# Kernel optimization log

Measured on AMD Instinct MI355X. Metric: run time of the kernel, lower is better.

## Reference

```python
import jax, jax.numpy as jnp
import numpy as np

N_NODES = 50000


def _gcn_conv(x, W, b, src, dst, n_nodes):
    """PyG GCNConv: add self-loops, symmetric deg^-1/2 norm, linear, aggregate, bias."""
    # add self-loops
    loop = jnp.arange(n_nodes, dtype=src.dtype)
    s = jnp.concatenate([src, loop])  # [E+N]
    d = jnp.concatenate([dst, loop])  # [E+N]
    # degree of A + I computed over targets
    deg = jax.ops.segment_sum(jnp.ones_like(d, dtype=x.dtype), d, num_segments=n_nodes)
    dinv = jnp.where(deg > 0, jax.lax.rsqrt(deg), 0.0)
    norm = dinv[s] * dinv[d]  # [E+N]
    h = x @ W  # [N, out] transform-first (in_dim >= out_dim friendly)
    msg = h[s] * norm[:, None]  # [E+N, out]
    out = jax.ops.segment_sum(msg, d, num_segments=n_nodes)
    return out + b


def setup_inputs() -> dict:
    key = jax.random.key(0)
    k1, k2, k3, k4 = jax.random.split(key, 4)
    in_dim, hidden, out_dim = 256, 128, 64
    E = 800000
    x = jax.random.normal(k1, (N_NODES, in_dim), dtype=jnp.float32)
    edge_index = jax.random.randint(k2, (2, E), 0, N_NODES, dtype=jnp.int64)
    W1 = jax.random.normal(k3, (in_dim, hidden), dtype=jnp.float32) / np.sqrt(in_dim)
    b1 = jnp.zeros((hidden,), dtype=jnp.float32)
    W2 = jax.random.normal(k4, (hidden, out_dim), dtype=jnp.float32) / np.sqrt(hidden)
    b2 = jnp.zeros((out_dim,), dtype=jnp.float32)
    return {"x": x, "edge_index": edge_index, "W1": W1, "b1": b1, "W2": W2, "b2": b2}


def reference(x, edge_index, W1, b1, W2, b2):
    src, dst = edge_index[0], edge_index[1]
    h = _gcn_conv(x, W1, b1, src, dst, N_NODES)
    h = jax.nn.relu(h)
    out = _gcn_conv(h, W2, b2, src, dst, N_NODES)
    return out
```

## Files before the change

kernel.cpp:

```cpp
#include <hip/hip_runtime.h>

#define N_NODES 50000
#define NCH 256
#define NBKT 256

typedef short bf16x8 __attribute__((ext_vector_type(8)));
typedef float f32x4 __attribute__((ext_vector_type(4)));

__device__ inline unsigned short f2bf(float f) {
    union { float f; unsigned u; } v; v.f = f;
    unsigned u = v.u;
    unsigned lsb = (u >> 16) & 1u;
    u += 0x7fffu + lsb;
    return (unsigned short)(u >> 16);
}

__device__ inline float bf2f(unsigned short h) {
    union { unsigned u; float f; } v; v.u = ((unsigned)h) << 16;
    return v.f;
}

__global__ __launch_bounds__(256) void prep(const int* __restrict__ dst,
                                            int* __restrict__ cnt, int E, int epc,
                                            const float* __restrict__ W1,
                                            const float* __restrict__ W2,
                                            unsigned short* __restrict__ B1h,
                                            unsigned short* __restrict__ B1l,
                                            unsigned short* __restrict__ B2h,
                                            unsigned short* __restrict__ B2l) {
    const int c = blockIdx.x;
    if (c < NCH) {
        __shared__ int h[NBKT];
        h[threadIdx.x] = 0;
        __syncthreads();
        const int e0 = c * epc;
        const int e1 = min(E, e0 + epc);
        for (int e = e0 + threadIdx.x; e < e1; e += 256)
            atomicAdd(&h[dst[e] >> 8], 1);
        __syncthreads();
        cnt[c * NBKT + threadIdx.x] = h[threadIdx.x];
        return;
    }
    int i = (c - NCH) * 256 + threadIdx.x;
    const float* W;
    unsigned short *Th, *Tl;
    int K, logM, idx;
    if (i < 32768) { W = W1; Th = B1h; Tl = B1l; K = 256; logM = 7; idx = i; }
    else if (i < 32768 + 8192) { W = W2; Th = B2h; Tl = B2l; K = 128; logM = 6; idx = i - 32768; }
    else return;
    const int M = 1 << logM;
    const int KS = K / 32;
    int k = idx >> logM;
    int n = idx & (M - 1);
    float v = W[idx];
    unsigned short h = f2bf(v);
    unsigned short l = f2bf(v - bf2f(h));
    int g = n >> 4, n16 = n & 15, ks = k >> 5, quad = (k >> 3) & 3, j = k & 7;
    size_t o = ((size_t)((g * KS + ks) * 64 + quad * 16 + n16)) * 8 + j;
    Th[o] = h;
    Tl[o] = l;
}

__global__ __launch_bounds__(256) void bkt_scan_chunks(const int* __restrict__ cnt,
                                                       int* __restrict__ off,
                                                       int* __restrict__ total) {
    __shared__ int sh[256];
    const int b = blockIdx.x;
    const int t = threadIdx.x;
    int v = cnt[t * NBKT + b];
    sh[t] = v;
    __syncthreads();
    for (int o = 1; o < 256; o <<= 1) {
        int u = (t >= o) ? sh[t - o] : 0;
        __syncthreads();
        sh[t] += u;
        __syncthreads();
    }
    off[t * NBKT + b] = sh[t] - v;
    if (t == 255) total[b] = sh[255];
}

__global__ __launch_bounds__(256) void bkt_scan_base(const int* __restrict__ total,
                                                     int* __restrict__ bbase,
                                                     int* __restrict__ rowptr,
                                                     int N, int E) {
    __shared__ int sh[256];
    const int t = threadIdx.x;
    int v = total[t];
    sh[t] = v;
    __syncthreads();
    for (int o = 1; o < 256; o <<= 1) {
        int u = (t >= o) ? sh[t - o] : 0;
        __syncthreads();
        sh[t] += u;
        __syncthreads();
    }
    bbase[t] = sh[t] - v;
    if (t == 255) bbase[256] = sh[255];
    if (t == 0) rowptr[N] = E;
}

__global__ __launch_bounds__(256) void bkt_scatter(const int* __restrict__ src,
                                                   const int* __restrict__ dst,
                                                   const int* __restrict__ off,
                                                   const int* __restrict__ bbase,
                                                   unsigned* __restrict__ pairs,
                                                   int E, int epc) {
    __shared__ int cur[NBKT];
    const int c = blockIdx.x;
    cur[threadIdx.x] = bbase[threadIdx.x] + off[c * NBKT + threadIdx.x];
    __syncthreads();
    const int e0 = c * epc;
    const int e1 = min(E, e0 + epc);
    for (int e = e0 + threadIdx.x; e < e1; e += 256) {
        int s = src[e];
        int d = dst[e];
        int pos = atomicAdd(&cur[d >> 8], 1);
        pairs[pos] = ((unsigned)s << 8) | (unsigned)(d & 255);
    }
}

__global__ __launch_bounds__(256) void bkt_csr(const unsigned* __restrict__ pairs,
                                               const int* __restrict__ bbase,
                                               int* __restrict__ rowptr,
                                               int* __restrict__ csr_src,
                                               float* __restrict__ dinv, int N) {
    __shared__ int lh[256];
    __shared__ int sc[256];
    __shared__ int lcur[256];
    const int b = blockIdx.x;
    const int t = threadIdx.x;
    const int ebase = bbase[b];
    const int eend = bbase[b + 1];
    const int node0 = b << 8;

    lh[t] = 0;
    __syncthreads();
    for (int e = ebase + t; e < eend; e += 256)
        atomicAdd(&lh[pairs[e] & 255u], 1);
    __syncthreads();
    int v = lh[t];
    sc[t] = v;
    __syncthreads();
    for (int o = 1; o < 256; o <<= 1) {
        int u = (t >= o) ? sc[t - o] : 0;
        __syncthreads();
        sc[t] += u;
        __syncthreads();
    }
    const int excl = sc[t] - v;
    lcur[t] = ebase + excl;
    const int node = node0 + t;
    if (node < N) {
        rowptr[node] = ebase + excl;
        dinv[node] = rsqrtf((float)(v + 1));
    }
    __syncthreads();
    for (int e = ebase + t; e < eend; e += 256) {
        unsigned p = pairs[e];
        int pos = atomicAdd(&lcur[p & 255u], 1);
        csr_src[pos] = (int)(p >> 8);
    }
}

template <int K, int M>
__global__ __launch_bounds__(M * 4) void gemm_mfma_v4(const float* __restrict__ A,
                                                      const unsigned short* __restrict__ Bfh,
                                                      const unsigned short* __restrict__ Bfl,
                                                      const float* __restrict__ dinv,
                                                      unsigned short* __restrict__ Cb, int N) {
    const int KS = K / 32;
    const int THREADS = M * 4;
    const int CPT = 512 / THREADS;
    const int PL = 64 * 40;
    const int CPAIRS = M / 32;

    __shared__ __align__(16) unsigned short Ah[2 * PL];
    __shared__ __align__(16) unsigned short Al[2 * PL];

    const int tid = threadIdx.x;
    const int wave = tid >> 6;
    const int lane = tid & 63;
    const int n16 = lane & 15;
    const int quad = lane >> 4;
    const int cpair = wave & (CPAIRS - 1);
    const int rpair = wave / CPAIRS;
    const int row0 = blockIdx.x * 64;

    bf16x8 bh[2][2], bl[2][2];
    auto loadB = [&](int ks, int par) {
#pragma unroll
        for (int ct = 0; ct < 2; ct++) {
            const int g = cpair * 2 + ct;
            const size_t o = ((size_t)(g * KS + ks) * 64 + lane) * 8;
            bh[par][ct] = *(const bf16x8*)(Bfh + o);
            bl[par][ct] = *(const bf16x8*)(Bfl + o);
        }
    };
    loadB(0, 0);

    int srow[CPT], sc4[CPT];
    const float* aptr[CPT];
#pragma unroll
    for (int p = 0; p < CPT; p++) {
        int q = p * THREADS + tid;
        srow[p] = q >> 3;
        sc4[p] = q & 7;
        int grow = row0 + srow[p];
        if (grow >= N) grow = N - 1;
        aptr[p] = A + (size_t)grow * K + sc4[p] * 4;
    }

    float4 pre[CPT];
#pragma unroll
    for (int p = 0; p < CPT; p++) pre[p] = *(const float4*)(aptr[p]);

#pragma unroll
    for (int p = 0; p < CPT; p++) {
        ushort4 h4, l4;
        unsigned short* hp = (unsigned short*)&h4;
        unsigned short* lp = (unsigned short*)&l4;
        float av[4] = {pre[p].x, pre[p].y, pre[p].z, pre[p].w};
#pragma unroll
        for (int j = 0; j < 4; j++) {
            unsigned short h = f2bf(av[j]);
            hp[j] = h;
            lp[j] = f2bf(av[j] - bf2f(h));
        }
        *(ushort4*)(Ah + srow[p] * 40 + sc4[p] * 4) = h4;
        *(ushort4*)(Al + srow[p] * 40 + sc4[p] * 4) = l4;
    }
    if (KS > 1) {
#pragma unroll
        for (int p = 0; p < CPT; p++) pre[p] = *(const float4*)(aptr[p] + 32);
    }
    __syncthreads();

    f32x4 acc[2][2] = {};

#pragma unroll
    for (int ks = 0; ks < KS; ks++) {
        const int cur = ks & 1;
        if (ks + 1 < KS) loadB(ks + 1, cur ^ 1);
#pragma unroll
        for (int rt = 0; rt < 2; rt++) {
            const int ro = cur * PL + (rpair * 32 + rt * 16 + n16) * 40 + quad * 8;
            bf16x8 ah = *(const bf16x8*)(Ah + ro);
            bf16x8 al = *(const bf16x8*)(Al + ro);
#pragma unroll
            for (int ct = 0; ct < 2; ct++) {
                acc[rt][ct] = __builtin_amdgcn_mfma_f32_16x16x32_bf16(ah, bh[cur][ct], acc[rt][ct], 0, 0, 0);
                acc[rt][ct] = __builtin_amdgcn_mfma_f32_16x16x32_bf16(ah, bl[cur][ct], acc[rt][ct], 0, 0, 0);
                acc[rt][ct] = __builtin_amdgcn_mfma_f32_16x16x32_bf16(al, bh[cur][ct], acc[rt][ct], 0, 0, 0);
            }
        }
        if (ks + 1 < KS) {
            const int nxt = (cur ^ 1) * PL;
#pragma unroll
            for (int p = 0; p < CPT; p++) {
                ushort4 h4, l4;
                unsigned short* hp = (unsigned short*)&h4;
                unsigned short* lp = (unsigned short*)&l4;
                float av[4] = {pre[p].x, pre[p].y, pre[p].z, pre[p].w};
#pragma unroll
                for (int j = 0; j < 4; j++) {
                    unsigned short h = f2bf(av[j]);
                    hp[j] = h;
                    lp[j] = f2bf(av[j] - bf2f(h));
                }
                *(ushort4*)(Ah + nxt + srow[p] * 40 + sc4[p] * 4) = h4;
                *(ushort4*)(Al + nxt + srow[p] * 40 + sc4[p] * 4) = l4;
            }
            if (ks + 2 < KS) {
#pragma unroll
                for (int p = 0; p < CPT; p++)
                    pre[p] = *(const float4*)(aptr[p] + (ks + 2) * 32);
            }
        }
        __syncthreads();
    }

#pragma unroll
    for (int rt = 0; rt < 2; rt++) {
#pragma unroll
        for (int ct = 0; ct < 2; ct++) {
            const int col = cpair * 32 + ct * 16 + n16;
            const int rbase = row0 + rpair * 32 + rt * 16 + quad * 4;
#pragma unroll
            for (int r = 0; r < 4; r++) {
                int orow = rbase + r;
                if (orow < N) {
                    Cb[(size_t)orow * M + col] = f2bf(dinv[orow] * acc[rt][ct][r]);
                }
            }
        }
    }
}

template <int K, int M>
__global__ __launch_bounds__(M * 4) void gemm_mfma_bfA(const unsigned short* __restrict__ A,
                                                       const unsigned short* __restrict__ Bfh,
                                                       const unsigned short* __restrict__ Bfl,
                                                       const float* __restrict__ dinv,
                                                       unsigned short* __restrict__ Cb, int N) {
    const int KS = K / 32;
    const int THREADS = M * 4;
    const int CPT = 256 / THREADS ? 256 / THREADS : 1;
    const int PL = 64 * 40;
    const int CPAIRS = M / 32;

    __shared__ __align__(16) unsigned short Ah[2 * PL];

    const int tid = threadIdx.x;
    const int wave = tid >> 6;
    const int lane = tid & 63;
    const int n16 = lane & 15;
    const int quad = lane >> 4;
    const int cpair = wave & (CPAIRS - 1);
    const int rpair = wave / CPAIRS;
    const int row0 = blockIdx.x * 64;

    bf16x8 bh[2][2], bl[2][2];
    auto loadB = [&](int ks, int par) {
#pragma unroll
        for (int ct = 0; ct < 2; ct++) {
            const int g = cpair * 2 + ct;
            const size_t o = ((size_t)(g * KS + ks) * 64 + lane) * 8;
            bh[par][ct] = *(const bf16x8*)(Bfh + o);
            bl[par][ct] = *(const bf16x8*)(Bfl + o);
        }
    };
    loadB(0, 0);

    const int srow = tid >> 2;
    const int sc8 = tid & 3;
    const unsigned short* aptr;
    {
        int grow = row0 + srow;
        if (grow >= N) grow = N - 1;
        aptr = A + (size_t)grow * K + sc8 * 8;
    }

    bf16x8 pre = *(const bf16x8*)(aptr);

    {
        ushort4* d0 = (ushort4*)(Ah + srow * 40 + sc8 * 8);
        ushort4 lo, hi;
        unsigned short* lp = (unsigned short*)&lo;
        unsigned short* hp = (unsigned short*)&hi;
#pragma unroll
        for (int j = 0; j < 4; j++) { lp[j] = (unsigned short)pre[j]; hp[j] = (unsigned short)pre[j + 4]; }
        d0[0] = lo;
        d0[1] = hi;
    }
    if (KS > 1) pre = *(const bf16x8*)(aptr + 32);
    __syncthreads();

    f32x4 acc[2][2] = {};

#pragma unroll
    for (int ks = 0; ks < KS; ks++) {
        const int cur = ks & 1;
        if (ks + 1 < KS) loadB(ks + 1, cur ^ 1);
#pragma unroll
        for (int rt = 0; rt < 2; rt++) {
            const int ro = cur * PL + (rpair * 32 + rt * 16 + n16) * 40 + quad * 8;
            bf16x8 ah = *(const bf16x8*)(Ah + ro);
#pragma unroll
            for (int ct = 0; ct < 2; ct++) {
                acc[rt][ct] = __builtin_amdgcn_mfma_f32_16x16x32_bf16(ah, bh[cur][ct], acc[rt][ct], 0, 0, 0);
                acc[rt][ct] = __builtin_amdgcn_mfma_f32_16x16x32_bf16(ah, bl[cur][ct], acc[rt][ct], 0, 0, 0);
            }
        }
        if (ks + 1 < KS) {
            const int nxt = (cur ^ 1) * PL;
            ushort4* d0 = (ushort4*)(Ah + nxt + srow * 40 + sc8 * 8);
            ushort4 lo, hi;
            unsigned short* lp = (unsigned short*)&lo;
            unsigned short* hp = (unsigned short*)&hi;
#pragma unroll
            for (int j = 0; j < 4; j++) { lp[j] = (unsigned short)pre[j]; hp[j] = (unsigned short)pre[j + 4]; }
            d0[0] = lo;
            d0[1] = hi;
            if (ks + 2 < KS) pre = *(const bf16x8*)(aptr + (ks + 2) * 32);
        }
        __syncthreads();
    }

#pragma unroll
    for (int rt = 0; rt < 2; rt++) {
#pragma unroll
        for (int ct = 0; ct < 2; ct++) {
            const int col = cpair * 32 + ct * 16 + n16;
            const int rbase = row0 + rpair * 32 + rt * 16 + quad * 4;
#pragma unroll
            for (int r = 0; r < 4; r++) {
                int orow = rbase + r;
                if (orow < N) {
                    Cb[(size_t)orow * M + col] = f2bf(dinv[orow] * acc[rt][ct][r]);
                }
            }
        }
    }
}

template <int M>
__global__ __launch_bounds__(256) void gather_to_bf16(const unsigned short* __restrict__ hnb,
                                                      const int* __restrict__ rowptr,
                                                      const int* __restrict__ csr_src,
                                                      const float* __restrict__ dinv,
                                                      const float* __restrict__ bias,
                                                      unsigned short* __restrict__ outp, int n) {
    const int MQ = M / 8;
    const int GPB = 256 / MQ;
    int g = blockIdx.x * GPB + threadIdx.x / MQ;
    int j = threadIdx.x % MQ;
    if (g >= n) return;

    float acc[8];
    {
        bf16x8 v = *(const bf16x8*)(hnb + (size_t)g * M + j * 8);
#pragma unroll
        for (int i = 0; i < 8; i++) acc[i] = bf2f((unsigned short)v[i]);
    }

    int e = rowptr[g];
    const int end = rowptr[g + 1];
    for (; e + 3 < end; e += 4) {
        int s0 = csr_src[e];
        int s1 = csr_src[e + 1];
        int s2 = csr_src[e + 2];
        int s3 = csr_src[e + 3];
        bf16x8 v0 = *(const bf16x8*)(hnb + (size_t)s0 * M + j * 8);
        bf16x8 v1 = *(const bf16x8*)(hnb + (size_t)s1 * M + j * 8);
        bf16x8 v2 = *(const bf16x8*)(hnb + (size_t)s2 * M + j * 8);
        bf16x8 v3 = *(const bf16x8*)(hnb + (size_t)s3 * M + j * 8);
#pragma unroll
        for (int i = 0; i < 8; i++) {
            acc[i] += (bf2f((unsigned short)v0[i]) + bf2f((unsigned short)v1[i])) +
                      (bf2f((unsigned short)v2[i]) + bf2f((unsigned short)v3[i]));
        }
    }
    for (; e < end; e++) {
        int s0 = csr_src[e];
        bf16x8 v0 = *(const bf16x8*)(hnb + (size_t)s0 * M + j * 8);
#pragma unroll
        for (int i = 0; i < 8; i++) acc[i] += bf2f((unsigned short)v0[i]);
    }

    const float s = dinv[g];
    bf16x8 r;
#pragma unroll
    for (int i = 0; i < 8; i++) {
        float t = fmaxf(s * acc[i] + bias[j * 8 + i], 0.0f);
        r[i] = (short)f2bf(t);
    }
    *(bf16x8*)(outp + (size_t)g * M + j * 8) = r;
}

template <int M>
__global__ __launch_bounds__(256) void gather_to_f32(const unsigned short* __restrict__ hnb,
                                                     const int* __restrict__ rowptr,
                                                     const int* __restrict__ csr_src,
                                                     const float* __restrict__ dinv,
                                                     const float* __restrict__ bias,
                                                     float* __restrict__ outp, int n) {
    const int MQ = M / 8;
    const int GPB = 256 / MQ;
    int g = blockIdx.x * GPB + threadIdx.x / MQ;
    int j = threadIdx.x % MQ;
    if (g >= n) return;

    float acc[8];
    {
        bf16x8 v = *(const bf16x8*)(hnb + (size_t)g * M + j * 8);
#pragma unroll
        for (int i = 0; i < 8; i++) acc[i] = bf2f((unsigned short)v[i]);
    }

    int e = rowptr[g];
    const int end = rowptr[g + 1];
    for (; e + 3 < end; e += 4) {
        int s0 = csr_src[e];
        int s1 = csr_src[e + 1];
        int s2 = csr_src[e + 2];
        int s3 = csr_src[e + 3];
        bf16x8 v0 = *(const bf16x8*)(hnb + (size_t)s0 * M + j * 8);
        bf16x8 v1 = *(const bf16x8*)(hnb + (size_t)s1 * M + j * 8);
        bf16x8 v2 = *(const bf16x8*)(hnb + (size_t)s2 * M + j * 8);
        bf16x8 v3 = *(const bf16x8*)(hnb + (size_t)s3 * M + j * 8);
#pragma unroll
        for (int i = 0; i < 8; i++) {
            acc[i] += (bf2f((unsigned short)v0[i]) + bf2f((unsigned short)v1[i])) +
                      (bf2f((unsigned short)v2[i]) + bf2f((unsigned short)v3[i]));
        }
    }
    for (; e < end; e++) {
        int s0 = csr_src[e];
        bf16x8 v0 = *(const bf16x8*)(hnb + (size_t)s0 * M + j * 8);
#pragma unroll
        for (int i = 0; i < 8; i++) acc[i] += bf2f((unsigned short)v0[i]);
    }

    const float s = dinv[g];
    float r[8];
#pragma unroll
    for (int i = 0; i < 8; i++) r[i] = s * acc[i] + bias[j * 8 + i];
    float* op = outp + (size_t)g * M + j * 8;
    *(float4*)(op) = make_float4(r[0], r[1], r[2], r[3]);
    *(float4*)(op + 4) = make_float4(r[4], r[5], r[6], r[7]);
}

extern "C" void kernel_launch(void* const* d_in, const int* in_sizes, int n_in,
                              void* d_out, int out_size, void* d_ws, size_t ws_size,
                              hipStream_t stream) {
    const float* x  = (const float*)d_in[0];
    const int*   ei = (const int*)d_in[1];
    const float* W1 = (const float*)d_in[2];
    const float* b1 = (const float*)d_in[3];
    const float* W2 = (const float*)d_in[4];
    const float* b2 = (const float*)d_in[5];

    const int N = N_NODES;
    const int E = in_sizes[1] / 2;
    const int* src = ei;
    const int* dst = ei + E;

    char* ws = (char*)d_ws;
    size_t off = 0;
    auto carve = [&](size_t bytes) {
        char* p = ws + off;
        off += (bytes + 255) & ~(size_t)255;
        return p;
    };
    int*      cnt     = (int*)     carve((size_t)NCH * NBKT * 4);
    int*      offm    = (int*)     carve((size_t)NCH * NBKT * 4);
    int*      total   = (int*)     carve((size_t)NBKT * 4);
    int*      bbase   = (int*)     carve((size_t)(NBKT + 1) * 4);
    unsigned* pairs   = (unsigned*)carve((size_t)E * 4);
    int*      rowptr  = (int*)     carve((size_t)(N + 1) * 4);
    int*      csr_src = (int*)     carve((size_t)E * 4);
    float*    dinv    = (float*)   carve((size_t)N * 4);
    unsigned short* W1th = (unsigned short*)carve((size_t)256 * 128 * 2);
    unsigned short* W1tl = (unsigned short*)carve((size_t)256 * 128 * 2);
    unsigned short* W2th = (unsigned short*)carve((size_t)128 * 64 * 2);
    unsigned short* W2tl = (unsigned short*)carve((size_t)128 * 64 * 2);
    unsigned short* hn1b = (unsigned short*)carve((size_t)N * 128 * 2);
    unsigned short* h1b  = (unsigned short*)carve((size_t)N * 128 * 2);
    unsigned short* hn2b = hn1b;

    const int epc = (E + NCH - 1) / NCH;
    const int nbk = (N + 255) >> 8;

    prep<<<NCH + 160, 256, 0, stream>>>(dst, cnt, E, epc, W1, W2, W1th, W1tl, W2th, W2tl);
    bkt_scan_chunks<<<NBKT, 256, 0, stream>>>(cnt, offm, total);
    bkt_scan_base<<<1, 256, 0, stream>>>(total, bbase, rowptr, N, E);
    bkt_scatter<<<NCH, 256, 0, stream>>>(src, dst, offm, bbase, pairs, E, epc);
    bkt_csr<<<nbk, 256, 0, stream>>>(pairs, bbase, rowptr, csr_src, dinv, N);

    const int GB = (N + 63) / 64;

    gemm_mfma_v4<256, 128><<<GB, 512, 0, stream>>>(x, W1th, W1tl, dinv, hn1b, N);
    {
        const int GPB = 256 / (128 / 8);
        gather_to_bf16<128><<<(N + GPB - 1) / GPB, 256, 0, stream>>>(
            hn1b, rowptr, csr_src, dinv, b1, h1b, N);
    }

    gemm_mfma_bfA<128, 64><<<GB, 256, 0, stream>>>(h1b, W2th, W2tl, dinv, hn2b, N);
    {
        const int GPB = 256 / (64 / 8);
        gather_to_f32<64><<<(N + GPB - 1) / GPB, 256, 0, stream>>>(
            hn2b, rowptr, csr_src, dinv, b2, (float*)d_out, N);
    }
}
```

Measured before the change: 196.7 us.

## Fuse layer-1 gather into layer-2 GEMM and fold bucket base scan into consumers

The layer-1 neighbour aggregation (with bias, ReLU and bf16 conversion) now runs inside the layer-2 MFMA GEMM. Each block gathers its 64 rows into shared memory and multiplies them directly, so the h1b intermediate is no longer written to or read back from global memory. The single-block bkt_scan_base kernel is also removed: bkt_scatter and bkt_csr each redo the 256-entry prefix scan locally, which saves launches at the cost of some redundant scan work. The fused kernel holds the whole K panel in shared memory, and its gather phase runs with only 64 rows per block, which may lower occupancy and latency hiding compared with the standalone gather.

```diff
diff --git a/kernel.cpp b/kernel.cpp
--- a/kernel.cpp
+++ b/kernel.cpp
@@ -80,11 +80,15 @@
     if (t == 255) total[b] = sh[255];
 }
 
-__global__ __launch_bounds__(256) void bkt_scan_base(const int* __restrict__ total,
-                                                     int* __restrict__ bbase,
-                                                     int* __restrict__ rowptr,
-                                                     int N, int E) {
+__global__ __launch_bounds__(256) void bkt_scatter(const int* __restrict__ src,
+                                                   const int* __restrict__ dst,
+                                                   const int* __restrict__ off,
+                                                   const int* __restrict__ total,
+                                                   unsigned* __restrict__ pairs,
+                                                   int E, int epc) {
     __shared__ int sh[256];
+    __shared__ int cur[NBKT];
+    const int c = blockIdx.x;
     const int t = threadIdx.x;
     int v = total[t];
     sh[t] = v;
@@ -95,24 +99,11 @@
         sh[t] += u;
         __syncthreads();
     }
-    bbase[t] = sh[t] - v;
-    if (t == 255) bbase[256] = sh[255];
-    if (t == 0) rowptr[N] = E;
-}
-
-__global__ __launch_bounds__(256) void bkt_scatter(const int* __restrict__ src,
-                                                   const int* __restrict__ dst,
-                                                   const int* __restrict__ off,
-                                                   const int* __restrict__ bbase,
-                                                   unsigned* __restrict__ pairs,
-                                                   int E, int epc) {
-    __shared__ int cur[NBKT];
-    const int c = blockIdx.x;
-    cur[threadIdx.x] = bbase[threadIdx.x] + off[c * NBKT + threadIdx.x];
+    cur[t] = (sh[t] - v) + off[c * NBKT + t];
     __syncthreads();
     const int e0 = c * epc;
     const int e1 = min(E, e0 + epc);
-    for (int e = e0 + threadIdx.x; e < e1; e += 256) {
+    for (int e = e0 + t; e < e1; e += 256) {
         int s = src[e];
         int d = dst[e];
         int pos = atomicAdd(&cur[d >> 8], 1);
@@ -121,7 +112,7 @@
 }
 
 __global__ __launch_bounds__(256) void bkt_csr(const unsigned* __restrict__ pairs,
-                                               const int* __restrict__ bbase,
+                                               const int* __restrict__ total,
                                                int* __restrict__ rowptr,
                                                int* __restrict__ csr_src,
                                                float* __restrict__ dinv, int N) {
@@ -130,8 +121,17 @@
     __shared__ int lcur[256];
     const int b = blockIdx.x;
     const int t = threadIdx.x;
-    const int ebase = bbase[b];
-    const int eend = bbase[b + 1];
+
+    sc[t] = total[t];
+    __syncthreads();
+    for (int o = 1; o < 256; o <<= 1) {
+        int u = (t >= o) ? sc[t - o] : 0;
+        __syncthreads();
+        sc[t] += u;
+        __syncthreads();
+    }
+    const int eend = sc[b];
+    const int ebase = eend - total[b];
     const int node0 = b << 8;
 
     lh[t] = 0;
@@ -151,9 +151,9 @@
     const int excl = sc[t] - v;
     lcur[t] = ebase + excl;
     const int node = node0 + t;
-    if (node < N) {
+    if (node <= N) {
         rowptr[node] = ebase + excl;
-        dinv[node] = rsqrtf((float)(v + 1));
+        if (node < N) dinv[node] = rsqrtf((float)(v + 1));
     }
     __syncthreads();
     for (int e = ebase + t; e < eend; e += 256) {
@@ -298,18 +298,19 @@
 }
 
 template <int K, int M>
-__global__ __launch_bounds__(M * 4) void gemm_mfma_bfA(const unsigned short* __restrict__ A,
-                                                       const unsigned short* __restrict__ Bfh,
-                                                       const unsigned short* __restrict__ Bfl,
-                                                       const float* __restrict__ dinv,
-                                                       unsigned short* __restrict__ Cb, int N) {
+__global__ __launch_bounds__(256) void gather_gemm2(const unsigned short* __restrict__ hnb,
+                                                    const int* __restrict__ rowptr,
+                                                    const int* __restrict__ csr_src,
+                                                    const float* __restrict__ dinv,
+                                                    const float* __restrict__ bias,
+                                                    const unsigned short* __restrict__ Bfh,
+                                                    const unsigned short* __restrict__ Bfl,
+                                                    unsigned short* __restrict__ Cb, int N) {
     const int KS = K / 32;
-    const int THREADS = M * 4;
-    const int CPT = 256 / THREADS ? 256 / THREADS : 1;
-    const int PL = 64 * 40;
     const int CPAIRS = M / 32;
-
-    __shared__ __align__(16) unsigned short Ah[2 * PL];
+    const int PLP = 64 * 40;
+
+    __shared__ __align__(16) unsigned short Ah[KS * PLP];
 
     const int tid = threadIdx.x;
     const int wave = tid >> 6;
@@ -332,39 +333,68 @@
     };
     loadB(0, 0);
 
-    const int srow = tid >> 2;
-    const int sc8 = tid & 3;
-    const unsigned short* aptr;
     {
-        int grow = row0 + srow;
-        if (grow >= N) grow = N - 1;
-        aptr = A + (size_t)grow * K + sc8 * 8;
-    }
-
-    bf16x8 pre = *(const bf16x8*)(aptr);
-
-    {
-        ushort4* d0 = (ushort4*)(Ah + srow * 40 + sc8 * 8);
-        ushort4 lo, hi;
-        unsigned short* lp = (unsigned short*)&lo;
-        unsigned short* hp = (unsigned short*)&hi;
-#pragma unroll
-        for (int j = 0; j < 4; j++) { lp[j] = (unsigned short)pre[j]; hp[j] = (unsigned short)pre[j + 4]; }
-        d0[0] = lo;
-        d0[1] = hi;
-    }
-    if (KS > 1) pre = *(const bf16x8*)(aptr + 32);
+        const int j = tid & 15;
+        const int nl = tid >> 4;
+        const int panel = j >> 2;
+        const int coff = (j & 3) * 8;
+#pragma unroll
+        for (int p = 0; p < 4; p++) {
+            const int r = p * 16 + nl;
+            const int g = row0 + r;
+            unsigned short* ldst = Ah + panel * PLP + r * 40 + coff;
+            if (g < N) {
+                float acc[8];
+                {
+                    bf16x8 v = *(const bf16x8*)(hnb + (size_t)g * K + j * 8);
+#pragma unroll
+                    for (int i = 0; i < 8; i++) acc[i] = bf2f((unsigned short)v[i]);
+                }
+                int e = rowptr[g];
+                const int end = rowptr[g + 1];
+                for (; e + 3 < end; e += 4) {
+                    int s0 = csr_src[e];
+                    int s1 = csr_src[e + 1];
+                    int s2 = csr_src[e + 2];
+                    int s3 = csr_src[e + 3];
+                    bf16x8 v0 = *(const bf16x8*)(hnb + (size_t)s0 * K + j * 8);
+                    bf16x8 v1 = *(const bf16x8*)(hnb + (size_t)s1 * K + j * 8);
+                    bf16x8 v2 = *(const bf16x8*)(hnb + (size_t)s2 * K + j * 8);
+                    bf16x8 v3 = *(const bf16x8*)(hnb + (size_t)s3 * K + j * 8);
+#pragma unroll
+                    for (int i = 0; i < 8; i++) {
+                        acc[i] += (bf2f((unsigned short)v0[i]) + bf2f((unsigned short)v1[i])) +
+                                  (bf2f((unsigned short)v2[i]) + bf2f((unsigned short)v3[i]));
+                    }
+                }
+                for (; e < end; e++) {
+                    int s0 = csr_src[e];
+                    bf16x8 v0 = *(const bf16x8*)(hnb + (size_t)s0 * K + j * 8);
+#pragma unroll
+                    for (int i = 0; i < 8; i++) acc[i] += bf2f((unsigned short)v0[i]);
+                }
+                const float s = dinv[g];
+                bf16x8 rr;
+#pragma unroll
+                for (int i = 0; i < 8; i++)
+                    rr[i] = (short)f2bf(fmaxf(s * acc[i] + bias[j * 8 + i], 0.0f));
+                *(bf16x8*)ldst = rr;
+            } else {
+                bf16x8 z = {};
+                *(bf16x8*)ldst = z;
+            }
+        }
+    }
     __syncthreads();
 
     f32x4 acc[2][2] = {};
-
 #pragma unroll
     for (int ks = 0; ks < KS; ks++) {
         const int cur = ks & 1;
         if (ks + 1 < KS) loadB(ks + 1, cur ^ 1);
 #pragma unroll
         for (int rt = 0; rt < 2; rt++) {
-            const int ro = cur * PL + (rpair * 32 + rt * 16 + n16) * 40 + quad * 8;
+            const int ro = ks * PLP + (rpair * 32 + rt * 16 + n16) * 40 + quad * 8;
             bf16x8 ah = *(const bf16x8*)(Ah + ro);
 #pragma unroll
             for (int ct = 0; ct < 2; ct++) {
@@ -372,19 +402,6 @@
                 acc[rt][ct] = __builtin_amdgcn_mfma_f32_16x16x32_bf16(ah, bl[cur][ct], acc[rt][ct], 0, 0, 0);
             }
         }
-        if (ks + 1 < KS) {
-            const int nxt = (cur ^ 1) * PL;
-            ushort4* d0 = (ushort4*)(Ah + nxt + srow * 40 + sc8 * 8);
-            ushort4 lo, hi;
-            unsigned short* lp = (unsigned short*)&lo;
-            unsigned short* hp = (unsigned short*)&hi;
-#pragma unroll
-            for (int j = 0; j < 4; j++) { lp[j] = (unsigned short)pre[j]; hp[j] = (unsigned short)pre[j + 4]; }
-            d0[0] = lo;
-            d0[1] = hi;
-            if (ks + 2 < KS) pre = *(const bf16x8*)(aptr + (ks + 2) * 32);
-        }
-        __syncthreads();
     }
 
 #pragma unroll
@@ -402,60 +419,6 @@
             }
         }
     }
-}
-
-template <int M>
-__global__ __launch_bounds__(256) void gather_to_bf16(const unsigned short* __restrict__ hnb,
-                                                      const int* __restrict__ rowptr,
-                                                      const int* __restrict__ csr_src,
-                                                      const float* __restrict__ dinv,
-                                                      const float* __restrict__ bias,
-                                                      unsigned short* __restrict__ outp, int n) {
-    const int MQ = M / 8;
-    const int GPB = 256 / MQ;
-    int g = blockIdx.x * GPB + threadIdx.x / MQ;
-    int j = threadIdx.x % MQ;
-    if (g >= n) return;
-
-    float acc[8];
-    {
-        bf16x8 v = *(const bf16x8*)(hnb + (size_t)g * M + j * 8);
-#pragma unroll
-        for (int i = 0; i < 8; i++) acc[i] = bf2f((unsigned short)v[i]);
-    }
-
-    int e = rowptr[g];
-    const int end = rowptr[g + 1];
-    for (; e + 3 < end; e += 4) {
-        int s0 = csr_src[e];
-        int s1 = csr_src[e + 1];
-        int s2 = csr_src[e + 2];
-        int s3 = csr_src[e + 3];
-        bf16x8 v0 = *(const bf16x8*)(hnb + (size_t)s0 * M + j * 8);
-        bf16x8 v1 = *(const bf16x8*)(hnb + (size_t)s1 * M + j * 8);
-        bf16x8 v2 = *(const bf16x8*)(hnb + (size_t)s2 * M + j * 8);
-        bf16x8 v3 = *(const bf16x8*)(hnb + (size_t)s3 * M + j * 8);
-#pragma unroll
-        for (int i = 0; i < 8; i++) {
-            acc[i] += (bf2f((unsigned short)v0[i]) + bf2f((unsigned short)v1[i])) +
-                      (bf2f((unsigned short)v2[i]) + bf2f((unsigned short)v3[i]));
-        }
-    }
-    for (; e < end; e++) {
-        int s0 = csr_src[e];
-        bf16x8 v0 = *(const bf16x8*)(hnb + (size_t)s0 * M + j * 8);
-#pragma unroll
-        for (int i = 0; i < 8; i++) acc[i] += bf2f((unsigned short)v0[i]);
-    }
-
-    const float s = dinv[g];
-    bf16x8 r;
-#pragma unroll
-    for (int i = 0; i < 8; i++) {
-        float t = fmaxf(s * acc[i] + bias[j * 8 + i], 0.0f);
-        r[i] = (short)f2bf(t);
-    }
-    *(bf16x8*)(outp + (size_t)g * M + j * 8) = r;
 }
 
 template <int M>
@@ -536,7 +499,6 @@
     int*      cnt     = (int*)     carve((size_t)NCH * NBKT * 4);
     int*      offm    = (int*)     carve((size_t)NCH * NBKT * 4);
     int*      total   = (int*)     carve((size_t)NBKT * 4);
-    int*      bbase   = (int*)     carve((size_t)(NBKT + 1) * 4);
     unsigned* pairs   = (unsigned*)carve((size_t)E * 4);
     int*      rowptr  = (int*)     carve((size_t)(N + 1) * 4);
     int*      csr_src = (int*)     carve((size_t)E * 4);
@@ -546,28 +508,23 @@
     unsigned short* W2th = (unsigned short*)carve((size_t)128 * 64 * 2);
     unsigned short* W2tl = (unsigned short*)carve((size_t)128 * 64 * 2);
     unsigned short* hn1b = (unsigned short*)carve((size_t)N * 128 * 2);
-    unsigned short* h1b  = (unsigned short*)carve((size_t)N * 128 * 2);
-    unsigned short* hn2b = hn1b;
+    unsigned short* hn2b = (unsigned short*)carve((size_t)N * 64 * 2);
 
     const int epc = (E + NCH - 1) / NCH;
     const int nbk = (N + 255) >> 8;
 
     prep<<<NCH + 160, 256, 0, stream>>>(dst, cnt, E, epc, W1, W2, W1th, W1tl, W2th, W2tl);
     bkt_scan_chunks<<<NBKT, 256, 0, stream>>>(cnt, offm, total);
-    bkt_scan_base<<<1, 256, 0, stream>>>(total, bbase, rowptr, N, E);
-    bkt_scatter<<<NCH, 256, 0, stream>>>(src, dst, offm, bbase, pairs, E, epc);
-    bkt_csr<<<nbk, 256, 0, stream>>>(pairs, bbase, rowptr, csr_src, dinv, N);
+    bkt_scatter<<<NCH, 256, 0, stream>>>(src, dst, offm, total, pairs, E, epc);
+    bkt_csr<<<nbk, 256, 0, stream>>>(pairs, total, rowptr, csr_src, dinv, N);
 
     const int GB = (N + 63) / 64;
 
     gemm_mfma_v4<256, 128><<<GB, 512, 0, stream>>>(x, W1th, W1tl, dinv, hn1b, N);
-    {
-        const int GPB = 256 / (128 / 8);
-        gather_to_bf16<128><<<(N + GPB - 1) / GPB, 256, 0, stream>>>(
-            hn1b, rowptr, csr_src, dinv, b1, h1b, N);
-    }
-
-    gemm_mfma_bfA<128, 64><<<GB, 256, 0, stream>>>(h1b, W2th, W2tl, dinv, hn2b, N);
+
+    gather_gemm2<128, 64><<<GB, 256, 0, stream>>>(hn1b, rowptr, csr_src, dinv, b1,
+                                                  W2th, W2tl, hn2b, N);
+
     {
         const int GPB = 256 / (64 / 8);
         gather_to_f32<64><<<(N + GPB - 1) / GPB, 256, 0, stream>>>(
```

Measured after the change: 198.5 us. About the same (+0.9%).
